# Optimization experiments

Hardware: AMD Instinct MI355X
Metric: run time of the kernel (lower is better)

## Reference

```python
import jax, jax.numpy as jnp
import numpy as np


def _gru_step(h, x, Wih, Whh, bih, bhh):
    # PyTorch GRU cell: gates ordered (r, z, n)
    gi = x @ Wih.T + bih
    gh = h @ Whh.T + bhh
    ir, iz, inn = jnp.split(gi, 3, axis=-1)
    hr, hz, hn = jnp.split(gh, 3, axis=-1)
    r = jax.nn.sigmoid(ir + hr)
    u = jax.nn.sigmoid(iz + hz)
    n = jnp.tanh(inn + r * hn)
    return (1.0 - u) * n + u * h


def _forward(mini_batch, eps, W_ih1, W_hh1, b_ih1, b_hh1, W_ih2, W_hh2, b_ih2, b_hh2,
             h1_0, h2_0, Wt1, bt1, Wloc, bloc, Wsc, bsc, We1, be1, We2, be2, We3, be3):
    B = mini_batch.shape[0]
    x_tbf = jnp.swapaxes(mini_batch, 0, 1)      # [T,B,dim_x]
    eps_tbf = jnp.swapaxes(eps, 0, 1)           # [T,B,dim_z]
    h2_init = jnp.broadcast_to(h2_0, (B, h2_0.shape[0]))
    h1_init = jnp.broadcast_to(h1_0, (B, h1_0.shape[0]))

    # gen_RNN_2 over full sequence (all seq_lengths == T, pack/pad is identity)
    def scan2(h, x):
        h = _gru_step(h, x, W_ih2, W_hh2, b_ih2, b_hh2)
        return h, h
    _, h2_seq = jax.lax.scan(scan2, h2_init, x_tbf)              # [T,B,dim_h2]
    # at step t the emitter sees h2_output[t-2] (h2_0 for t==1): shift right by one
    h2_shift = jnp.concatenate([h2_init[None], h2_seq[:-1]], axis=0)

    def step(h1, inp):
        eps_t, h2_t = inp
        # stoch_trans (dz): MLP -> z_loc, z_scale
        hid = jax.nn.relu(h1 @ Wt1.T + bt1)
        z_loc = hid @ Wloc.T + bloc
        z_scale = jax.nn.softplus(hid @ Wsc.T + bsc)
        z_t = z_loc + z_scale * eps_t                            # reparameterized sample
        h1n = _gru_step(h1, z_t, W_ih1, W_hh1, b_ih1, b_hh1)     # gen_RNN_1 one step
        dx_in = jnp.concatenate([h1n, h2_t], axis=-1)            # [B, dim_h1+dim_h2]
        e = jax.nn.relu(dx_in @ We1.T + be1)                     # emitter (dx)
        e = jax.nn.relu(e @ We2.T + be2)
        x_ps = jax.nn.sigmoid(e @ We3.T + be3)                   # Bernoulli probs
        return h1n, x_ps

    _, xps = jax.lax.scan(step, h1_init, (eps_tbf, h2_shift))    # [T,B,dim_x]
    return jnp.swapaxes(xps, 0, 1)                               # [B,T,dim_x]


def setup_inputs() -> dict:
    key = jax.random.key(0)
    B, T = 256, 1000
    DX, DZ, H1, H2, DDX, DDZ = 100, 100, 10, 10, 20, 20
    ks = jax.random.split(key, 24)
    f32 = jnp.float32
    w = lambda k, shape: (jax.random.normal(k, shape, f32) * 0.1)
    inp = {
        "mini_batch": (jax.random.uniform(ks[0], (B, T, DX)) < 0.5).astype(f32),
        "eps": jax.random.normal(ks[1], (B, T, DZ), f32),
        # gen_RNN_1: input dim_z -> hidden dim_h1
        "W_ih1": w(ks[2], (3 * H1, DZ)), "W_hh1": w(ks[3], (3 * H1, H1)),
        "b_ih1": w(ks[4], (3 * H1,)), "b_hh1": w(ks[5], (3 * H1,)),
        # gen_RNN_2: input dim_x -> hidden dim_h2
        "W_ih2": w(ks[6], (3 * H2, DX)), "W_hh2": w(ks[7], (3 * H2, H2)),
        "b_ih2": w(ks[8], (3 * H2,)), "b_hh2": w(ks[9], (3 * H2,)),
        "h1_0": jnp.zeros((H1,), f32), "h2_0": jnp.zeros((H2,), f32),
        # stoch_trans (dz): dim_h1 -> dim_dz -> (dim_z loc, dim_z scale)
        "Wt1": w(ks[10], (DDZ, H1)), "bt1": w(ks[11], (DDZ,)),
        "Wloc": w(ks[12], (DZ, DDZ)), "bloc": w(ks[13], (DZ,)),
        "Wsc": w(ks[14], (DZ, DDZ)), "bsc": w(ks[15], (DZ,)),
        # emitter (dx): (dim_h1+dim_h2) -> dim_dx -> dim_dx -> dim_x, sigmoid
        "We1": w(ks[16], (DDX, H1 + H2)), "be1": w(ks[17], (DDX,)),
        "We2": w(ks[18], (DDX, DDX)), "be2": w(ks[19], (DDX,)),
        "We3": w(ks[20], (DX, DDX)), "be3": w(ks[21], (DX,)),
    }
    return inp


def reference(mini_batch, eps, W_ih1, W_hh1, b_ih1, b_hh1, W_ih2, W_hh2, b_ih2, b_hh2,
              h1_0, h2_0, Wt1, bt1, Wloc, bloc, Wsc, bsc, We1, be1, We2, be2, We3, be3):
    return _forward(mini_batch, eps, W_ih1, W_hh1, b_ih1, b_hh1, W_ih2, W_hh2, b_ih2, b_hh2,
                    h1_0, h2_0, Wt1, bt1, Wloc, bloc, Wsc, bsc, We1, be1, We2, be2, We3, be3)
```

## Files before the change

### kernel.cpp

```cpp
#include <hip/hip_runtime.h>
#include <cstdint>

#define T_LEN 1000
#define NB    256

__device__ __forceinline__ float rcpf_(float x)     { return __builtin_amdgcn_rcpf(x); }
__device__ __forceinline__ float sigmoidf_(float x) { return rcpf_(1.f + __expf(-x)); }
__device__ __forceinline__ float tanhf_(float x) {
    float e = __expf(2.f * x);
    return 1.f - 2.f * rcpf_(e + 1.f);
}
__device__ __forceinline__ float softplusf_(float x) {
    return fmaxf(x, 0.f) + __logf(1.f + __expf(-fabsf(x)));
}
__device__ __forceinline__ float bcast_(float v, int l) {
    return __uint_as_float(__builtin_amdgcn_readlane(__float_as_uint(v), l));
}

#define BARRIER_SYNC() asm volatile("s_waitcnt lgkmcnt(0)\n\ts_barrier" ::: "memory")

__global__ __launch_bounds__(256) void gi2_kernel(
    const float* __restrict__ x, const float* __restrict__ W,
    const float* __restrict__ bias, float* __restrict__ out)
{
    __shared__ float xsT[100 * 67];

    const int tid = threadIdx.x;
    const int64_t base = (int64_t)blockIdx.x * (64 * 100);
    const float4* gx = (const float4*)(x + base);

#pragma unroll
    for (int it = 0; it < 7; ++it) {
        int i = tid + it * 256;
        if (i < 1600) {
            int r  = i / 25;
            int k4 = i - r * 25;
            float4 v = gx[i];
            xsT[(4 * k4 + 0) * 67 + r] = v.x;
            xsT[(4 * k4 + 1) * 67 + r] = v.y;
            xsT[(4 * k4 + 2) * 67 + r] = v.z;
            xsT[(4 * k4 + 3) * 67 + r] = v.w;
        }
    }
    __syncthreads();

    const int lane = tid & 63;
    const int wv   = __builtin_amdgcn_readfirstlane(tid >> 6);
    const int j0   = wv * 8;

    float acc[8];
#pragma unroll
    for (int jj = 0; jj < 8; ++jj) acc[jj] = 0.f;

    for (int k = 0; k < 100; ++k) {
        float xv = xsT[k * 67 + lane];
#pragma unroll
        for (int jj = 0; jj < 8; ++jj) {
            int j = j0 + jj; j = j > 29 ? 29 : j;
            acc[jj] = fmaf(xv, W[j * 100 + k], acc[jj]);
        }
    }
    float* orow = out + base + (int64_t)lane * 100;
#pragma unroll
    for (int jj = 0; jj < 8; ++jj) {
        int j = j0 + jj;
        if (j < 30) orow[j] = acc[jj] + bias[j];
    }
}

__global__ __launch_bounds__(128) void scan_kernel(
    const float* __restrict__ eps,
    const float* __restrict__ W_ih1, const float* __restrict__ W_hh1,
    const float* __restrict__ b_ih1, const float* __restrict__ b_hh1,
    const float* __restrict__ W_hh2, const float* __restrict__ b_hh2,
    const float* __restrict__ h1_0,  const float* __restrict__ h2_0,
    const float* __restrict__ Wt1,   const float* __restrict__ bt1,
    const float* __restrict__ Wloc,  const float* __restrict__ bloc,
    const float* __restrict__ Wsc,   const float* __restrict__ bsc,
    const float* __restrict__ We1,   const float* __restrict__ be1,
    const float* __restrict__ We2,   const float* __restrict__ be2,
    const float* __restrict__ We3,   const float* __restrict__ be3,
    float* out)
{
    __shared__ __align__(16) float ss2[2][52];
    __shared__ __align__(16) float sh1ring[2][12];

    const int lane = threadIdx.x & 63;
    const int64_t rowbase = (int64_t)blockIdx.x * T_LEN * 100;
    const int wave = __builtin_amdgcn_readfirstlane((int)(threadIdx.x >> 6));

    if (wave == 0) {
        const int j  = lane & 31;
        const int jc = j < 30 ? j : 29;
        const int h  = lane >> 5;
        const int lt = lane < 20 ? lane : 19;
        const int ls = lane < 50 ? lane : 49;

        float wt1r[10], whh1r[10], wscA[20], wscB[20], wbig[52], Cr[20];
#pragma unroll
        for (int k = 0; k < 10; ++k) {
            wt1r[k]  = Wt1[lt * 10 + k];
            whh1r[k] = W_hh1[jc * 10 + k];
        }
        float bt1r  = bt1[lt];
        float bhh1r = b_hh1[jc];
        float br1   = b_ih1[jc];
#pragma unroll
        for (int l = 0; l < 20; ++l) {
            wscA[l] = Wsc[ls * 20 + l];
            wscB[l] = Wsc[(ls + 50) * 20 + l];
        }
        float bscA = bsc[ls], bscB = bsc[ls + 50];
#pragma unroll
        for (int i = 0; i < 50; ++i) wbig[i] = W_ih1[jc * 100 + h * 50 + i];
        wbig[50] = 0.f; wbig[51] = 0.f;

        float dr = 0.f;
#pragma unroll
        for (int l = 0; l < 20; ++l) Cr[l] = 0.f;
        for (int kk = 0; kk < 100; ++kk) {
            float w = W_ih1[jc * 100 + kk];
            dr = fmaf(w, bloc[kk], dr);
#pragma unroll
            for (int l = 0; l < 20; ++l) Cr[l] = fmaf(w, Wloc[kk * 20 + l], Cr[l]);
        }

        if (lane < 2) { ss2[0][50 + lane] = 0.f; ss2[1][50 + lane] = 0.f; }

        float h1keep = h1_0[lane < 10 ? lane : 0];
        float sh1_[10];
#pragma unroll
        for (int k = 0; k < 10; ++k) sh1_[k] = h1_0[k];

        const float* erow = eps + rowbase;
        float eA0 = erow[ls],        eB0 = erow[ls + 50];
        float eA1 = erow[100 + ls],  eB1 = erow[100 + ls + 50];

#pragma unroll 1
        for (int t = 0; t <= T_LEN; ++t) {
            if (t < T_LEN) {
                const int tp = t + 2 < T_LEN ? t + 2 : T_LEN - 1;
                float eAf = erow[(int64_t)tp * 100 + ls];
                float eBf = erow[(int64_t)tp * 100 + ls + 50];

                float ha = bt1r, hb = 0.f, ga = bhh1r, gb = 0.f;
#pragma unroll
                for (int k = 0; k < 5; ++k) {
                    ha = fmaf(wt1r[2 * k],      sh1_[2 * k],     ha);
                    hb = fmaf(wt1r[2 * k + 1],  sh1_[2 * k + 1], hb);
                    ga = fmaf(whh1r[2 * k],     sh1_[2 * k],     ga);
                    gb = fmaf(whh1r[2 * k + 1], sh1_[2 * k + 1], gb);
                }
                float hidv = fmaxf(ha + hb, 0.f);
                float gh1v = ga + gb;

                float sgh[20];
#pragma unroll
                for (int l = 0; l < 20; ++l) sgh[l] = bcast_(hidv, l);

                float sA0 = bscA, sA1 = 0.f, sB0 = bscB, sB1 = 0.f, q0 = dr, q1 = 0.f;
#pragma unroll
                for (int l = 0; l < 10; ++l) {
                    sA0 = fmaf(wscA[2 * l],     sgh[2 * l],     sA0);
                    sA1 = fmaf(wscA[2 * l + 1], sgh[2 * l + 1], sA1);
                    sB0 = fmaf(wscB[2 * l],     sgh[2 * l],     sB0);
                    sB1 = fmaf(wscB[2 * l + 1], sgh[2 * l + 1], sB1);
                    q0  = fmaf(Cr[2 * l],       sgh[2 * l],     q0);
                    q1  = fmaf(Cr[2 * l + 1],   sgh[2 * l + 1], q1);
                }
                float gq = q0 + q1;
                float zA = softplusf_(sA0 + sA1) * eA0;
                float zB = softplusf_(sB0 + sB1) * eB0;
                if (lane < 50) { ss2[0][lane] = zA; ss2[1][lane] = zB; }

                eA0 = eA1; eB0 = eB1; eA1 = eAf; eB1 = eBf;

                __builtin_amdgcn_wave_barrier();

                const float4* sp4 = (const float4*)(&ss2[h][0]);
                float p0 = 0.f, p1 = 0.f, p2 = 0.f, p3 = 0.f;
#pragma unroll
                for (int c = 0; c < 13; ++c) {
                    float4 v = sp4[c];
                    p0 = fmaf(wbig[4 * c + 0], v.x, p0);
                    p1 = fmaf(wbig[4 * c + 1], v.y, p1);
                    p2 = fmaf(wbig[4 * c + 2], v.z, p2);
                    p3 = fmaf(wbig[4 * c + 3], v.w, p3);
                }
                float p = (p0 + p1) + (p2 + p3);
                float gi1v = p + __shfl_xor(p, 32) + br1 + gq;
                float av   = gi1v + gh1v;
                float a10  = __shfl(av,   lane + 10);
                float gin  = __shfl(gi1v, lane + 20);
                float ghn  = __shfl(gh1v, lane + 20);
                if (lane < 10) {
                    float r = sigmoidf_(av);
                    float u = sigmoidf_(a10);
                    float n = tanhf_(fmaf(r, ghn, gin));
                    h1keep = fmaf(u, h1keep - n, n);
                    sh1ring[t & 1][lane] = h1keep;
                }
#pragma unroll
                for (int k = 0; k < 10; ++k) sh1_[k] = bcast_(h1keep, k);
            }
            BARRIER_SYNC();
        }
    } else {
        const int lt20 = lane < 20 ? lane : 19;
        const int l30  = lane < 30 ? lane : 29;
        const int ls   = lane < 50 ? lane : 49;

        float whh2r[10];
#pragma unroll
        for (int k = 0; k < 10; ++k) whh2r[k] = W_hh2[l30 * 10 + k];
        float bhh2r = b_hh2[l30];

        float we1r[20], we2r[20], we3A[20], we3B[20];
#pragma unroll
        for (int k = 0; k < 20; ++k) {
            we1r[k] = We1[lt20 * 20 + k];
            we2r[k] = We2[lt20 * 20 + k];
            we3A[k] = We3[ls * 20 + k];
            we3B[k] = We3[(ls + 50) * 20 + k];
        }
        float be1r = be1[lt20], be2r = be2[lt20];
        float be3A = be3[ls],   be3B = be3[ls + 50];

        float h2keep = h2_0[lane < 10 ? lane : 0];
        float g2c[10], g2p[10];
#pragma unroll
        for (int k = 0; k < 10; ++k) { g2c[k] = h2_0[k]; g2p[k] = h2_0[k]; }

        float gcur = out[rowbase + l30];
        float gnxt = out[rowbase + 100 + l30];

#pragma unroll 1
        for (int t = 0; t <= T_LEN; ++t) {
            const int tp = t + 2 < T_LEN ? t + 2 : T_LEN - 1;
            float gfut = out[rowbase + (int64_t)tp * 100 + l30];

            float4 d0 = make_float4(0.f, 0.f, 0.f, 0.f);
            float4 d1 = d0; float d8 = 0.f, d9 = 0.f;
            if (t >= 1) {
                const int s1 = (t - 1) & 1;
                d0 = *(const float4*)(&sh1ring[s1][0]);
                d1 = *(const float4*)(&sh1ring[s1][4]);
                d8 = sh1ring[s1][8]; d9 = sh1ring[s1][9];
            }

            const bool upd = (t < T_LEN);
            if (upd) {
                float ga = bhh2r, gb = 0.f;
#pragma unroll
                for (int k = 0; k < 5; ++k) {
                    ga = fmaf(whh2r[2 * k],     g2c[2 * k],     ga);
                    gb = fmaf(whh2r[2 * k + 1], g2c[2 * k + 1], gb);
                }
                float gh2v = ga + gb;
                float gi2v = gcur;
                gcur = gnxt; gnxt = gfut;
                float a2  = gi2v + gh2v;
                float a10 = __shfl(a2,   lane + 10);
                float gin = __shfl(gi2v, lane + 20);
                float ghn = __shfl(gh2v, lane + 20);
                if (lane < 10) {
                    float r = sigmoidf_(a2);
                    float u = sigmoidf_(a10);
                    float n = tanhf_(fmaf(r, ghn, gin));
                    h2keep = fmaf(u, h2keep - n, n);
                }
            }

            if (t >= 1) {
                float ea = be1r, eb = 0.f;
                ea = fmaf(we1r[0], d0.x, ea); eb = fmaf(we1r[1], d0.y, eb);
                ea = fmaf(we1r[2], d0.z, ea); eb = fmaf(we1r[3], d0.w, eb);
                ea = fmaf(we1r[4], d1.x, ea); eb = fmaf(we1r[5], d1.y, eb);
                ea = fmaf(we1r[6], d1.z, ea); eb = fmaf(we1r[7], d1.w, eb);
                ea = fmaf(we1r[8], d8,   ea); eb = fmaf(we1r[9], d9,   eb);
#pragma unroll
                for (int k = 0; k < 5; ++k) {
                    ea = fmaf(we1r[10 + 2 * k],     g2p[2 * k],     ea);
                    eb = fmaf(we1r[10 + 2 * k + 1], g2p[2 * k + 1], eb);
                }
                float e1v = fmaxf(ea + eb, 0.f);

                float se1v[20];
#pragma unroll
                for (int l = 0; l < 20; ++l) se1v[l] = bcast_(e1v, l);

                float fa = be2r, fb = 0.f;
#pragma unroll
                for (int k = 0; k < 10; ++k) {
                    fa = fmaf(we2r[2 * k],     se1v[2 * k],     fa);
                    fb = fmaf(we2r[2 * k + 1], se1v[2 * k + 1], fb);
                }
                float e2v = fmaxf(fa + fb, 0.f);

                float se2v[20];
#pragma unroll
                for (int l = 0; l < 20; ++l) se2v[l] = bcast_(e2v, l);

                float xa0 = be3A, xa1 = 0.f, xb0 = be3B, xb1 = 0.f;
#pragma unroll
                for (int l = 0; l < 10; ++l) {
                    xa0 = fmaf(we3A[2 * l],     se2v[2 * l],     xa0);
                    xa1 = fmaf(we3A[2 * l + 1], se2v[2 * l + 1], xa1);
                    xb0 = fmaf(we3B[2 * l],     se2v[2 * l],     xb0);
                    xb1 = fmaf(we3B[2 * l + 1], se2v[2 * l + 1], xb1);
                }
                float xA = sigmoidf_(xa0 + xa1);
                float xB = sigmoidf_(xb0 + xb1);
                if (lane < 50) {
                    int64_t ro = rowbase + (int64_t)(t - 1) * 100;
                    out[ro + lane]      = xA;
                    out[ro + lane + 50] = xB;
                }
            }

            if (upd) {
#pragma unroll
                for (int k = 0; k < 10; ++k) g2p[k] = g2c[k];
#pragma unroll
                for (int k = 0; k < 10; ++k) g2c[k] = bcast_(h2keep, k);
            }
            BARRIER_SYNC();
        }
    }
}

extern "C" void kernel_launch(void* const* d_in, const int* in_sizes, int n_in,
                              void* d_out, int out_size, void* d_ws, size_t ws_size,
                              hipStream_t stream) {
    const float* mini_batch = (const float*)d_in[0];
    const float* eps        = (const float*)d_in[1];
    const float* W_ih1      = (const float*)d_in[2];
    const float* W_hh1      = (const float*)d_in[3];
    const float* b_ih1      = (const float*)d_in[4];
    const float* b_hh1      = (const float*)d_in[5];
    const float* W_ih2      = (const float*)d_in[6];
    const float* W_hh2      = (const float*)d_in[7];
    const float* b_ih2      = (const float*)d_in[8];
    const float* b_hh2      = (const float*)d_in[9];
    const float* h1_0       = (const float*)d_in[10];
    const float* h2_0       = (const float*)d_in[11];
    const float* Wt1        = (const float*)d_in[12];
    const float* bt1        = (const float*)d_in[13];
    const float* Wloc       = (const float*)d_in[14];
    const float* bloc       = (const float*)d_in[15];
    const float* Wsc        = (const float*)d_in[16];
    const float* bsc        = (const float*)d_in[17];
    const float* We1        = (const float*)d_in[18];
    const float* be1        = (const float*)d_in[19];
    const float* We2        = (const float*)d_in[20];
    const float* be2        = (const float*)d_in[21];
    const float* We3        = (const float*)d_in[22];
    const float* be3        = (const float*)d_in[23];
    float* out = (float*)d_out;

    gi2_kernel<<<(NB * T_LEN) / 64, 256, 0, stream>>>(mini_batch, W_ih2, b_ih2, out);

    scan_kernel<<<NB, 128, 0, stream>>>(eps, W_ih1, W_hh1, b_ih1, b_hh1, W_hh2, b_hh2,
                                        h1_0, h2_0, Wt1, bt1, Wloc, bloc, Wsc, bsc,
                                        We1, be1, We2, be2, We3, be3, out);
}
```

Measured before the change: 834.0 us.

## Add producer wave that prefetches eps and gi2 into LDS ring buffer

```diff
diff --git a/kernel.cpp b/kernel.cpp
--- a/kernel.cpp
+++ b/kernel.cpp
@@ -18,6 +18,13 @@
 }
 
 #define BARRIER_SYNC() asm volatile("s_waitcnt lgkmcnt(0)\n\ts_barrier" ::: "memory")
+
+__device__ __forceinline__ void gload_lds(const float* g, float* l) {
+    __builtin_amdgcn_global_load_lds(
+        (const __attribute__((address_space(1))) uint32_t*)g,
+        (__attribute__((address_space(3))) uint32_t*)l,
+        4, 0, 0);
+}
 
 __global__ __launch_bounds__(256) void gi2_kernel(
     const float* __restrict__ x, const float* __restrict__ W,
@@ -68,7 +75,7 @@
     }
 }
 
-__global__ __launch_bounds__(128) void scan_kernel(
+__global__ __launch_bounds__(192) void scan_kernel(
     const float* __restrict__ eps,
     const float* __restrict__ W_ih1, const float* __restrict__ W_hh1,
     const float* __restrict__ b_ih1, const float* __restrict__ b_hh1,
@@ -82,6 +89,7 @@
     const float* __restrict__ We3,   const float* __restrict__ be3,
     float* out)
 {
+    __shared__ __align__(16) float ring[4][192];
     __shared__ __align__(16) float ss2[2][52];
     __shared__ __align__(16) float sh1ring[2][12];
 
@@ -132,16 +140,14 @@
 #pragma unroll
         for (int k = 0; k < 10; ++k) sh1_[k] = h1_0[k];
 
-        const float* erow = eps + rowbase;
-        float eA0 = erow[ls],        eB0 = erow[ls + 50];
-        float eA1 = erow[100 + ls],  eB1 = erow[100 + ls + 50];
+        BARRIER_SYNC();
 
 #pragma unroll 1
         for (int t = 0; t <= T_LEN; ++t) {
             if (t < T_LEN) {
-                const int tp = t + 2 < T_LEN ? t + 2 : T_LEN - 1;
-                float eAf = erow[(int64_t)tp * 100 + ls];
-                float eBf = erow[(int64_t)tp * 100 + ls + 50];
+                const int slot = t & 3;
+                float eA = ring[slot][ls];
+                float eB = ring[slot][ls + 50];
 
                 float ha = bt1r, hb = 0.f, ga = bhh1r, gb = 0.f;
 #pragma unroll
@@ -169,11 +175,9 @@
                     q1  = fmaf(Cr[2 * l + 1],   sgh[2 * l + 1], q1);
                 }
                 float gq = q0 + q1;
-                float zA = softplusf_(sA0 + sA1) * eA0;
-                float zB = softplusf_(sB0 + sB1) * eB0;
+                float zA = softplusf_(sA0 + sA1) * eA;
+                float zB = softplusf_(sB0 + sB1) * eB;
                 if (lane < 50) { ss2[0][lane] = zA; ss2[1][lane] = zB; }
-
-                eA0 = eA1; eB0 = eB1; eA1 = eAf; eB1 = eBf;
 
                 __builtin_amdgcn_wave_barrier();
 
@@ -205,7 +209,7 @@
             }
             BARRIER_SYNC();
         }
-    } else {
+    } else if (wave == 1) {
         const int lt20 = lane < 20 ? lane : 19;
         const int l30  = lane < 30 ? lane : 29;
         const int ls   = lane < 50 ? lane : 49;
@@ -231,13 +235,13 @@
 #pragma unroll
         for (int k = 0; k < 10; ++k) { g2c[k] = h2_0[k]; g2p[k] = h2_0[k]; }
 
-        float gcur = out[rowbase + l30];
-        float gnxt = out[rowbase + 100 + l30];
+        BARRIER_SYNC();
 
 #pragma unroll 1
         for (int t = 0; t <= T_LEN; ++t) {
-            const int tp = t + 2 < T_LEN ? t + 2 : T_LEN - 1;
-            float gfut = out[rowbase + (int64_t)tp * 100 + l30];
+            const bool upd = (t < T_LEN);
+            float gi2v = 0.f;
+            if (upd) gi2v = ring[t & 3][128 + l30];
 
             float4 d0 = make_float4(0.f, 0.f, 0.f, 0.f);
             float4 d1 = d0; float d8 = 0.f, d9 = 0.f;
@@ -248,7 +252,6 @@
                 d8 = sh1ring[s1][8]; d9 = sh1ring[s1][9];
             }
 
-            const bool upd = (t < T_LEN);
             if (upd) {
                 float ga = bhh2r, gb = 0.f;
 #pragma unroll
@@ -257,8 +260,6 @@
                     gb = fmaf(whh2r[2 * k + 1], g2c[2 * k + 1], gb);
                 }
                 float gh2v = ga + gb;
-                float gi2v = gcur;
-                gcur = gnxt; gnxt = gfut;
                 float a2  = gi2v + gh2v;
                 float a10 = __shfl(a2,   lane + 10);
                 float gin = __shfl(gi2v, lane + 20);
@@ -324,6 +325,35 @@
 #pragma unroll
                 for (int k = 0; k < 10; ++k) g2c[k] = bcast_(h2keep, k);
             }
+            BARRIER_SYNC();
+        }
+    } else {
+        const float* erow = eps + rowbase;
+        const float* grow = out + rowbase;
+        const int le2 = 64 + (lane < 36 ? lane : 35);
+        const int lg  = lane < 30 ? lane : 29;
+
+#pragma unroll
+        for (int t0 = 0; t0 < 3; ++t0) {
+            const float* ep = erow + (int64_t)t0 * 100;
+            const float* gp = grow + (int64_t)t0 * 100;
+            gload_lds(ep + lane, &ring[t0][0]);
+            gload_lds(ep + le2,  &ring[t0][64]);
+            gload_lds(gp + lg,   &ring[t0][128]);
+        }
+        asm volatile("s_waitcnt vmcnt(6)" ::: "memory");
+        BARRIER_SYNC();
+
+#pragma unroll 1
+        for (int t = 0; t <= T_LEN; ++t) {
+            const int tp   = (t + 3 < T_LEN) ? t + 3 : T_LEN - 1;
+            const int slot = (t + 3) & 3;
+            const float* ep = erow + (int64_t)tp * 100;
+            const float* gp = grow + (int64_t)tp * 100;
+            gload_lds(ep + lane, &ring[slot][0]);
+            gload_lds(ep + le2,  &ring[slot][64]);
+            gload_lds(gp + lg,   &ring[slot][128]);
+            asm volatile("s_waitcnt vmcnt(6)" ::: "memory");
             BARRIER_SYNC();
         }
     }
@@ -360,7 +390,7 @@
 
     gi2_kernel<<<(NB * T_LEN) / 64, 256, 0, stream>>>(mini_batch, W_ih2, b_ih2, out);
 
-    scan_kernel<<<NB, 128, 0, stream>>>(eps, W_ih1, W_hh1, b_ih1, b_hh1, W_hh2, b_hh2,
+    scan_kernel<<<NB, 192, 0, stream>>>(eps, W_ih1, W_hh1, b_ih1, b_hh1, W_hh2, b_hh2,
                                         h1_0, h2_0, Wt1, bt1, Wloc, bloc, Wsc, bsc,
                                         We1, be1, We2, be2, We3, be3, out);
 }
```

After: 948.5 us. 13.7% more time.

## Move emitter MLP out of scan into a separate parallel kernel

Applied to the files above, without the earlier changes.

```diff
diff --git a/kernel.cpp b/kernel.cpp
--- a/kernel.cpp
+++ b/kernel.cpp
@@ -16,8 +16,6 @@
 __device__ __forceinline__ float bcast_(float v, int l) {
     return __uint_as_float(__builtin_amdgcn_readlane(__float_as_uint(v), l));
 }
-
-#define BARRIER_SYNC() asm volatile("s_waitcnt lgkmcnt(0)\n\ts_barrier" ::: "memory")
 
 __global__ __launch_bounds__(256) void gi2_kernel(
     const float* __restrict__ x, const float* __restrict__ W,
@@ -68,6 +66,102 @@
     }
 }
 
+
+#define H1_STEP(T, EA, EB, P)                                            \
+    do {                                                                 \
+        float ha = bt1r, hb = 0.f, ga = bhh1r, gb = 0.f;                 \
+        _Pragma("unroll")                                                \
+        for (int k_ = 0; k_ < 5; ++k_) {                                 \
+            ha = fmaf(wt1r[2*k_],    sh1_[2*k_],   ha);                  \
+            hb = fmaf(wt1r[2*k_+1],  sh1_[2*k_+1], hb);                  \
+            ga = fmaf(whh1r[2*k_],   sh1_[2*k_],   ga);                  \
+            gb = fmaf(whh1r[2*k_+1], sh1_[2*k_+1], gb);                  \
+        }                                                                \
+        float hidv = fmaxf(ha + hb, 0.f);                                \
+        float gh1v = ga + gb;                                            \
+        float sgh[20];                                                   \
+        _Pragma("unroll")                                                \
+        for (int l_ = 0; l_ < 20; ++l_) sgh[l_] = bcast_(hidv, l_);      \
+        float sA0 = bscA, sA1 = 0.f, sB0 = bscB, sB1 = 0.f;              \
+        float q0 = dr, q1 = 0.f;                                         \
+        _Pragma("unroll")                                                \
+        for (int l_ = 0; l_ < 10; ++l_) {                                \
+            sA0 = fmaf(wscA[2*l_],   sgh[2*l_],   sA0);                  \
+            sA1 = fmaf(wscA[2*l_+1], sgh[2*l_+1], sA1);                  \
+            sB0 = fmaf(wscB[2*l_],   sgh[2*l_],   sB0);                  \
+            sB1 = fmaf(wscB[2*l_+1], sgh[2*l_+1], sB1);                  \
+            q0  = fmaf(Cr[2*l_],     sgh[2*l_],   q0);                   \
+            q1  = fmaf(Cr[2*l_+1],   sgh[2*l_+1], q1);                   \
+        }                                                                \
+        float gq = q0 + q1;                                              \
+        float zA = softplusf_(sA0 + sA1) * (EA);                         \
+        float zB = softplusf_(sB0 + sB1) * (EB);                         \
+        if (lane < 50) { ss2[P][lane] = zA; ss2[P][52 + lane] = zB; }    \
+        {             \
+            int tp_ = (T) + 2 < T_LEN ? (T) + 2 : (T);                   \
+            const float* ep_ = erow + (int64_t)tp_ * 100;                \
+            (EA) = ep_[ls]; (EB) = ep_[ls + 50];                         \
+        }                                                                \
+        __builtin_amdgcn_wave_barrier();                                 \
+        {                                                                \
+            const float4* sp4_ = (const float4*)(&ss2[P][52 * h]);       \
+            float p0 = 0.f, p1 = 0.f, p2 = 0.f, p3 = 0.f;                \
+            _Pragma("unroll")                                            \
+            for (int c_ = 0; c_ < 13; ++c_) {                            \
+                float4 v_ = sp4_[c_];                                    \
+                p0 = fmaf(wbig[4*c_+0], v_.x, p0);                       \
+                p1 = fmaf(wbig[4*c_+1], v_.y, p1);                       \
+                p2 = fmaf(wbig[4*c_+2], v_.z, p2);                       \
+                p3 = fmaf(wbig[4*c_+3], v_.w, p3);                       \
+            }                                                            \
+            float p_ = (p0 + p1) + (p2 + p3);                            \
+            float gi1v = p_ + __shfl_xor(p_, 32) + br1 + gq;             \
+            float av   = gi1v + gh1v;                                    \
+            float a10  = __shfl(av,   lane + 10);                        \
+            float gin  = __shfl(gi1v, lane + 20);                        \
+            float ghn  = __shfl(gh1v, lane + 20);                        \
+            if (lane < 10) {                                             \
+                float r_ = sigmoidf_(av);                                \
+                float u_ = sigmoidf_(a10);                               \
+                float n_ = tanhf_(fmaf(r_, ghn, gin));                   \
+                h1keep = fmaf(u_, h1keep - n_, n_);                      \
+                out[rowbase + (int64_t)(T) * 100 + 30 + lane] = h1keep;  \
+            }                                                            \
+        }                                                                \
+        _Pragma("unroll")                                                \
+        for (int k_ = 0; k_ < 10; ++k_) sh1_[k_] = bcast_(h1keep, k_);   \
+    } while (0)
+
+#define H2_STEP(T, GC)                                                   \
+    do {                                                                 \
+        if (lane < 10)                 \
+            out[rowbase + (int64_t)(T) * 100 + 40 + lane] = h2keep;      \
+        float ga = bhh2r, gb = 0.f;                                      \
+        _Pragma("unroll")                                                \
+        for (int k_ = 0; k_ < 5; ++k_) {                                 \
+            ga = fmaf(whh2r[2*k_],   g2c[2*k_],   ga);                   \
+            gb = fmaf(whh2r[2*k_+1], g2c[2*k_+1], gb);                   \
+        }                                                                \
+        float gh2v = ga + gb;                                            \
+        float gi2v = (GC);                                               \
+        {                                         \
+            int tp_ = (T) + 2 < T_LEN ? (T) + 2 : (T);                   \
+            (GC) = out[rowbase + (int64_t)tp_ * 100 + l30];              \
+        }                                                                \
+        float a2  = gi2v + gh2v;                                         \
+        float a10 = __shfl(a2,   lane + 10);                             \
+        float gin = __shfl(gi2v, lane + 20);                             \
+        float ghn = __shfl(gh2v, lane + 20);                             \
+        if (lane < 10) {                                                 \
+            float r_ = sigmoidf_(a2);                                    \
+            float u_ = sigmoidf_(a10);                                   \
+            float n_ = tanhf_(fmaf(r_, ghn, gin));                       \
+            h2keep = fmaf(u_, h2keep - n_, n_);                          \
+        }                                                                \
+        _Pragma("unroll")                                                \
+        for (int k_ = 0; k_ < 10; ++k_) g2c[k_] = bcast_(h2keep, k_);    \
+    } while (0)
+
 __global__ __launch_bounds__(128) void scan_kernel(
     const float* __restrict__ eps,
     const float* __restrict__ W_ih1, const float* __restrict__ W_hh1,
@@ -77,13 +171,9 @@
     const float* __restrict__ Wt1,   const float* __restrict__ bt1,
     const float* __restrict__ Wloc,  const float* __restrict__ bloc,
     const float* __restrict__ Wsc,   const float* __restrict__ bsc,
-    const float* __restrict__ We1,   const float* __restrict__ be1,
-    const float* __restrict__ We2,   const float* __restrict__ be2,
-    const float* __restrict__ We3,   const float* __restrict__ be3,
     float* out)
 {
-    __shared__ __align__(16) float ss2[2][52];
-    __shared__ __align__(16) float sh1ring[2][12];
+    __shared__ __align__(16) float ss2[2][104];
 
     const int lane = threadIdx.x & 63;
     const int64_t rowbase = (int64_t)blockIdx.x * T_LEN * 100;
@@ -125,7 +215,10 @@
             for (int l = 0; l < 20; ++l) Cr[l] = fmaf(w, Wloc[kk * 20 + l], Cr[l]);
         }
 
-        if (lane < 2) { ss2[0][50 + lane] = 0.f; ss2[1][50 + lane] = 0.f; }
+        if (lane < 2) {
+            ss2[0][50 + lane] = 0.f; ss2[0][102 + lane] = 0.f;
+            ss2[1][50 + lane] = 0.f; ss2[1][102 + lane] = 0.f;
+        }
 
         float h1keep = h1_0[lane < 10 ? lane : 0];
         float sh1_[10];
@@ -137,194 +230,105 @@
         float eA1 = erow[100 + ls],  eB1 = erow[100 + ls + 50];
 
 #pragma unroll 1
-        for (int t = 0; t <= T_LEN; ++t) {
-            if (t < T_LEN) {
-                const int tp = t + 2 < T_LEN ? t + 2 : T_LEN - 1;
-                float eAf = erow[(int64_t)tp * 100 + ls];
-                float eBf = erow[(int64_t)tp * 100 + ls + 50];
-
-                float ha = bt1r, hb = 0.f, ga = bhh1r, gb = 0.f;
-#pragma unroll
-                for (int k = 0; k < 5; ++k) {
-                    ha = fmaf(wt1r[2 * k],      sh1_[2 * k],     ha);
-                    hb = fmaf(wt1r[2 * k + 1],  sh1_[2 * k + 1], hb);
-                    ga = fmaf(whh1r[2 * k],     sh1_[2 * k],     ga);
-                    gb = fmaf(whh1r[2 * k + 1], sh1_[2 * k + 1], gb);
-                }
-                float hidv = fmaxf(ha + hb, 0.f);
-                float gh1v = ga + gb;
-
-                float sgh[20];
-#pragma unroll
-                for (int l = 0; l < 20; ++l) sgh[l] = bcast_(hidv, l);
-
-                float sA0 = bscA, sA1 = 0.f, sB0 = bscB, sB1 = 0.f, q0 = dr, q1 = 0.f;
-#pragma unroll
-                for (int l = 0; l < 10; ++l) {
-                    sA0 = fmaf(wscA[2 * l],     sgh[2 * l],     sA0);
-                    sA1 = fmaf(wscA[2 * l + 1], sgh[2 * l + 1], sA1);
-                    sB0 = fmaf(wscB[2 * l],     sgh[2 * l],     sB0);
-                    sB1 = fmaf(wscB[2 * l + 1], sgh[2 * l + 1], sB1);
-                    q0  = fmaf(Cr[2 * l],       sgh[2 * l],     q0);
-                    q1  = fmaf(Cr[2 * l + 1],   sgh[2 * l + 1], q1);
-                }
-                float gq = q0 + q1;
-                float zA = softplusf_(sA0 + sA1) * eA0;
-                float zB = softplusf_(sB0 + sB1) * eB0;
-                if (lane < 50) { ss2[0][lane] = zA; ss2[1][lane] = zB; }
-
-                eA0 = eA1; eB0 = eB1; eA1 = eAf; eB1 = eBf;
-
-                __builtin_amdgcn_wave_barrier();
-
-                const float4* sp4 = (const float4*)(&ss2[h][0]);
-                float p0 = 0.f, p1 = 0.f, p2 = 0.f, p3 = 0.f;
-#pragma unroll
-                for (int c = 0; c < 13; ++c) {
-                    float4 v = sp4[c];
-                    p0 = fmaf(wbig[4 * c + 0], v.x, p0);
-                    p1 = fmaf(wbig[4 * c + 1], v.y, p1);
-                    p2 = fmaf(wbig[4 * c + 2], v.z, p2);
-                    p3 = fmaf(wbig[4 * c + 3], v.w, p3);
-                }
-                float p = (p0 + p1) + (p2 + p3);
-                float gi1v = p + __shfl_xor(p, 32) + br1 + gq;
-                float av   = gi1v + gh1v;
-                float a10  = __shfl(av,   lane + 10);
-                float gin  = __shfl(gi1v, lane + 20);
-                float ghn  = __shfl(gh1v, lane + 20);
-                if (lane < 10) {
-                    float r = sigmoidf_(av);
-                    float u = sigmoidf_(a10);
-                    float n = tanhf_(fmaf(r, ghn, gin));
-                    h1keep = fmaf(u, h1keep - n, n);
-                    sh1ring[t & 1][lane] = h1keep;
-                }
-#pragma unroll
-                for (int k = 0; k < 10; ++k) sh1_[k] = bcast_(h1keep, k);
-            }
-            BARRIER_SYNC();
+        for (int t = 0; t < T_LEN; t += 2) {
+            H1_STEP(t,     eA0, eB0, 0);
+            H1_STEP(t + 1, eA1, eB1, 1);
         }
     } else {
-        const int lt20 = lane < 20 ? lane : 19;
-        const int l30  = lane < 30 ? lane : 29;
-        const int ls   = lane < 50 ? lane : 49;
+        const int l30 = lane < 30 ? lane : 29;
 
         float whh2r[10];
 #pragma unroll
         for (int k = 0; k < 10; ++k) whh2r[k] = W_hh2[l30 * 10 + k];
         float bhh2r = b_hh2[l30];
 
-        float we1r[20], we2r[20], we3A[20], we3B[20];
-#pragma unroll
-        for (int k = 0; k < 20; ++k) {
-            we1r[k] = We1[lt20 * 20 + k];
-            we2r[k] = We2[lt20 * 20 + k];
-            we3A[k] = We3[ls * 20 + k];
-            we3B[k] = We3[(ls + 50) * 20 + k];
-        }
-        float be1r = be1[lt20], be2r = be2[lt20];
-        float be3A = be3[ls],   be3B = be3[ls + 50];
-
         float h2keep = h2_0[lane < 10 ? lane : 0];
-        float g2c[10], g2p[10];
-#pragma unroll
-        for (int k = 0; k < 10; ++k) { g2c[k] = h2_0[k]; g2p[k] = h2_0[k]; }
-
-        float gcur = out[rowbase + l30];
-        float gnxt = out[rowbase + 100 + l30];
+        float g2c[10];
+#pragma unroll
+        for (int k = 0; k < 10; ++k) g2c[k] = h2_0[k];
+
+        float gU = out[rowbase + l30];
+        float gV = out[rowbase + 100 + l30];
 
 #pragma unroll 1
-        for (int t = 0; t <= T_LEN; ++t) {
-            const int tp = t + 2 < T_LEN ? t + 2 : T_LEN - 1;
-            float gfut = out[rowbase + (int64_t)tp * 100 + l30];
-
-            float4 d0 = make_float4(0.f, 0.f, 0.f, 0.f);
-            float4 d1 = d0; float d8 = 0.f, d9 = 0.f;
-            if (t >= 1) {
-                const int s1 = (t - 1) & 1;
-                d0 = *(const float4*)(&sh1ring[s1][0]);
-                d1 = *(const float4*)(&sh1ring[s1][4]);
-                d8 = sh1ring[s1][8]; d9 = sh1ring[s1][9];
-            }
-
-            const bool upd = (t < T_LEN);
-            if (upd) {
-                float ga = bhh2r, gb = 0.f;
-#pragma unroll
-                for (int k = 0; k < 5; ++k) {
-                    ga = fmaf(whh2r[2 * k],     g2c[2 * k],     ga);
-                    gb = fmaf(whh2r[2 * k + 1], g2c[2 * k + 1], gb);
-                }
-                float gh2v = ga + gb;
-                float gi2v = gcur;
-                gcur = gnxt; gnxt = gfut;
-                float a2  = gi2v + gh2v;
-                float a10 = __shfl(a2,   lane + 10);
-                float gin = __shfl(gi2v, lane + 20);
-                float ghn = __shfl(gh2v, lane + 20);
-                if (lane < 10) {
-                    float r = sigmoidf_(a2);
-                    float u = sigmoidf_(a10);
-                    float n = tanhf_(fmaf(r, ghn, gin));
-                    h2keep = fmaf(u, h2keep - n, n);
-                }
-            }
-
-            if (t >= 1) {
-                float ea = be1r, eb = 0.f;
-                ea = fmaf(we1r[0], d0.x, ea); eb = fmaf(we1r[1], d0.y, eb);
-                ea = fmaf(we1r[2], d0.z, ea); eb = fmaf(we1r[3], d0.w, eb);
-                ea = fmaf(we1r[4], d1.x, ea); eb = fmaf(we1r[5], d1.y, eb);
-                ea = fmaf(we1r[6], d1.z, ea); eb = fmaf(we1r[7], d1.w, eb);
-                ea = fmaf(we1r[8], d8,   ea); eb = fmaf(we1r[9], d9,   eb);
-#pragma unroll
-                for (int k = 0; k < 5; ++k) {
-                    ea = fmaf(we1r[10 + 2 * k],     g2p[2 * k],     ea);
-                    eb = fmaf(we1r[10 + 2 * k + 1], g2p[2 * k + 1], eb);
-                }
-                float e1v = fmaxf(ea + eb, 0.f);
-
-                float se1v[20];
-#pragma unroll
-                for (int l = 0; l < 20; ++l) se1v[l] = bcast_(e1v, l);
-
-                float fa = be2r, fb = 0.f;
-#pragma unroll
-                for (int k = 0; k < 10; ++k) {
-                    fa = fmaf(we2r[2 * k],     se1v[2 * k],     fa);
-                    fb = fmaf(we2r[2 * k + 1], se1v[2 * k + 1], fb);
-                }
-                float e2v = fmaxf(fa + fb, 0.f);
-
-                float se2v[20];
-#pragma unroll
-                for (int l = 0; l < 20; ++l) se2v[l] = bcast_(e2v, l);
-
-                float xa0 = be3A, xa1 = 0.f, xb0 = be3B, xb1 = 0.f;
-#pragma unroll
-                for (int l = 0; l < 10; ++l) {
-                    xa0 = fmaf(we3A[2 * l],     se2v[2 * l],     xa0);
-                    xa1 = fmaf(we3A[2 * l + 1], se2v[2 * l + 1], xa1);
-                    xb0 = fmaf(we3B[2 * l],     se2v[2 * l],     xb0);
-                    xb1 = fmaf(we3B[2 * l + 1], se2v[2 * l + 1], xb1);
-                }
-                float xA = sigmoidf_(xa0 + xa1);
-                float xB = sigmoidf_(xb0 + xb1);
-                if (lane < 50) {
-                    int64_t ro = rowbase + (int64_t)(t - 1) * 100;
-                    out[ro + lane]      = xA;
-                    out[ro + lane + 50] = xB;
-                }
-            }
-
-            if (upd) {
-#pragma unroll
-                for (int k = 0; k < 10; ++k) g2p[k] = g2c[k];
-#pragma unroll
-                for (int k = 0; k < 10; ++k) g2c[k] = bcast_(h2keep, k);
-            }
-            BARRIER_SYNC();
+        for (int t = 0; t < T_LEN; t += 2) {
+            H2_STEP(t,     gU);
+            H2_STEP(t + 1, gV);
+        }
+    }
+}
+
+__global__ __launch_bounds__(256) void emit_kernel(
+    const float* __restrict__ We1, const float* __restrict__ be1,
+    const float* __restrict__ We2, const float* __restrict__ be2,
+    const float* __restrict__ We3, const float* __restrict__ be3,
+    float* out)
+{
+    const int lane = threadIdx.x & 63;
+    const int wid  = threadIdx.x >> 6;
+    const int lt = lane < 20 ? lane : 19;
+    const int ls = lane < 50 ? lane : 49;
+
+    float we1r[20], we2r[20], we3A[20], we3B[20];
+#pragma unroll
+    for (int k = 0; k < 20; ++k) {
+        we1r[k] = We1[lt * 20 + k];
+        we2r[k] = We2[lt * 20 + k];
+        we3A[k] = We3[ls * 20 + k];
+        we3B[k] = We3[(ls + 50) * 20 + k];
+    }
+    float be1r = be1[lt], be2r = be2[lt];
+    float be3A = be3[ls], be3B = be3[ls + 50];
+
+    const int64_t row0 = ((int64_t)blockIdx.x * 4 + wid) * 8;
+
+#pragma unroll 1
+    for (int rr = 0; rr < 8; ++rr) {
+        const int64_t r = row0 + rr;
+        float hvin = 0.f;
+        if (lane < 20) hvin = out[r * 100 + 30 + lane];
+
+        float hall[20];
+#pragma unroll
+        for (int l = 0; l < 20; ++l) hall[l] = bcast_(hvin, l);
+
+        float ea = be1r, eb = 0.f;
+#pragma unroll
+        for (int k = 0; k < 10; ++k) {
+            ea = fmaf(we1r[2 * k],     hall[2 * k],     ea);
+            eb = fmaf(we1r[2 * k + 1], hall[2 * k + 1], eb);
+        }
+        float e1v = fmaxf(ea + eb, 0.f);
+
+        float se1[20];
+#pragma unroll
+        for (int l = 0; l < 20; ++l) se1[l] = bcast_(e1v, l);
+
+        float fa = be2r, fb = 0.f;
+#pragma unroll
+        for (int k = 0; k < 10; ++k) {
+            fa = fmaf(we2r[2 * k],     se1[2 * k],     fa);
+            fb = fmaf(we2r[2 * k + 1], se1[2 * k + 1], fb);
+        }
+        float e2v = fmaxf(fa + fb, 0.f);
+
+        float se2[20];
+#pragma unroll
+        for (int l = 0; l < 20; ++l) se2[l] = bcast_(e2v, l);
+
+        float xa0 = be3A, xa1 = 0.f, xb0 = be3B, xb1 = 0.f;
+#pragma unroll
+        for (int l = 0; l < 10; ++l) {
+            xa0 = fmaf(we3A[2 * l],     se2[2 * l],     xa0);
+            xa1 = fmaf(we3A[2 * l + 1], se2[2 * l + 1], xa1);
+            xb0 = fmaf(we3B[2 * l],     se2[2 * l],     xb0);
+            xb1 = fmaf(we3B[2 * l + 1], se2[2 * l + 1], xb1);
+        }
+        float xA = sigmoidf_(xa0 + xa1);
+        float xB = sigmoidf_(xb0 + xb1);
+        if (lane < 50) {
+            out[r * 100 + lane]      = xA;
+            out[r * 100 + lane + 50] = xB;
         }
     }
 }
@@ -361,6 +365,7 @@
     gi2_kernel<<<(NB * T_LEN) / 64, 256, 0, stream>>>(mini_batch, W_ih2, b_ih2, out);
 
     scan_kernel<<<NB, 128, 0, stream>>>(eps, W_ih1, W_hh1, b_ih1, b_hh1, W_hh2, b_hh2,
-                                        h1_0, h2_0, Wt1, bt1, Wloc, bloc, Wsc, bsc,
-                                        We1, be1, We2, be2, We3, be3, out);
-}
+                                        h1_0, h2_0, Wt1, bt1, Wloc, bloc, Wsc, bsc, out);
+
+    emit_kernel<<<(NB * T_LEN) / 32, 256, 0, stream>>>(We1, be1, We2, be2, We3, be3, out);
+}
```

Result: no change. 832.8 us (-0.1%).

## Unroll GRU scan by two, shorten critical path with permlane swap and earlier sigmoid

Applied to the files above, without the earlier changes.

```diff
diff --git a/kernel.cpp b/kernel.cpp
--- a/kernel.cpp
+++ b/kernel.cpp
@@ -16,8 +16,12 @@
 __device__ __forceinline__ float bcast_(float v, int l) {
     return __uint_as_float(__builtin_amdgcn_readlane(__float_as_uint(v), l));
 }
-
-#define BARRIER_SYNC() asm volatile("s_waitcnt lgkmcnt(0)\n\ts_barrier" ::: "memory")
+__device__ __forceinline__ float halfsum_(float p) {
+    float a = p, b = p;
+    asm volatile("s_nop 1\n\tv_permlane32_swap_b32 %0, %1\n\ts_nop 1"
+                 : "+v"(a), "+v"(b));
+    return a + b;
+}
 
 __global__ __launch_bounds__(256) void gi2_kernel(
     const float* __restrict__ x, const float* __restrict__ W,
@@ -67,6 +71,86 @@
         if (j < 30) orow[j] = acc[jj] + bias[j];
     }
 }
+
+
+#define H1_STEP(T, EA, EB)                                               \
+    do {                                                                 \
+                                                \
+        float ha = bt1r, hb = 0.f;                                       \
+        _Pragma("unroll")                                                \
+        for (int k_ = 0; k_ < 5; ++k_) {                                 \
+            ha = fmaf(wt1r[2*k_],   sh1_[2*k_],   ha);                   \
+            hb = fmaf(wt1r[2*k_+1], sh1_[2*k_+1], hb);                   \
+        }                                                                \
+        float hidv = fmaxf(ha + hb, 0.f);                                \
+        float sgh[20];                                                   \
+        _Pragma("unroll")                                                \
+        for (int l_ = 0; l_ < 20; ++l_) sgh[l_] = bcast_(hidv, l_);      \
+                          \
+        float sA0 = bscA, sA1 = 0.f, sA2 = 0.f, sA3 = 0.f;               \
+        float sB0 = bscB, sB1 = 0.f, sB2 = 0.f, sB3 = 0.f;               \
+        float q0 = dr, q1 = 0.f, q2 = 0.f, q3 = 0.f;                     \
+        _Pragma("unroll")                                                \
+        for (int l_ = 0; l_ < 5; ++l_) {                                 \
+            sA0 = fmaf(wscA[4*l_],   sgh[4*l_],   sA0);                  \
+            sA1 = fmaf(wscA[4*l_+1], sgh[4*l_+1], sA1);                  \
+            sA2 = fmaf(wscA[4*l_+2], sgh[4*l_+2], sA2);                  \
+            sA3 = fmaf(wscA[4*l_+3], sgh[4*l_+3], sA3);                  \
+            sB0 = fmaf(wscB[4*l_],   sgh[4*l_],   sB0);                  \
+            sB1 = fmaf(wscB[4*l_+1], sgh[4*l_+1], sB1);                  \
+            sB2 = fmaf(wscB[4*l_+2], sgh[4*l_+2], sB2);                  \
+            sB3 = fmaf(wscB[4*l_+3], sgh[4*l_+3], sB3);                  \
+            q0  = fmaf(Cr[4*l_],     sgh[4*l_],   q0);                   \
+            q1  = fmaf(Cr[4*l_+1],   sgh[4*l_+1], q1);                   \
+            q2  = fmaf(Cr[4*l_+2],   sgh[4*l_+2], q2);                   \
+            q3  = fmaf(Cr[4*l_+3],   sgh[4*l_+3], q3);                   \
+        }                                                                \
+        float gq = (q0 + q1) + (q2 + q3);                                \
+        float zA = softplusf_((sA0 + sA1) + (sA2 + sA3)) * (EA);         \
+        float zB = softplusf_((sB0 + sB1) + (sB2 + sB3)) * (EB);         \
+        if (lane < 50) { ss2[lane] = zA; ss2[52 + lane] = zB; }          \
+          \
+        float ga = bhh1r, gb = 0.f;                                      \
+        _Pragma("unroll")                                                \
+        for (int k_ = 0; k_ < 5; ++k_) {                                 \
+            ga = fmaf(whh1r[2*k_],   sh1_[2*k_],   ga);                  \
+            gb = fmaf(whh1r[2*k_+1], sh1_[2*k_+1], gb);                  \
+        }                                                                \
+        float gh1v = ga + gb;                                            \
+        {                                                                \
+            int tp_ = (T) + 2 < T_LEN ? (T) + 2 : (T);                   \
+            const float* ep_ = erow + (int64_t)tp_ * 100;                \
+            (EA) = ep_[ls]; (EB) = ep_[ls + 50];                         \
+        }                                                                \
+        __builtin_amdgcn_wave_barrier();                                 \
+           \
+        {                                                                \
+            const float4* sp4_ = (const float4*)(&ss2[52 * h]);          \
+            float p0 = 0.f, p1 = 0.f, p2 = 0.f, p3 = 0.f;                \
+            _Pragma("unroll")                                            \
+            for (int c_ = 0; c_ < 13; ++c_) {                            \
+                float4 v_ = sp4_[c_];                                    \
+                p0 = fmaf(wbig[4*c_+0], v_.x, p0);                       \
+                p1 = fmaf(wbig[4*c_+1], v_.y, p1);                       \
+                p2 = fmaf(wbig[4*c_+2], v_.z, p2);                       \
+                p3 = fmaf(wbig[4*c_+3], v_.w, p3);                       \
+            }                                                            \
+            float p_ = (p0 + p1) + (p2 + p3);                            \
+            float gi1v = halfsum_(p_) + br1 + gq;                        \
+            float av   = gi1v + gh1v;                                    \
+            float sg   = sigmoidf_(av);          \
+            float su   = __shfl(sg,   lane + 10);                        \
+            float gin  = __shfl(gi1v, lane + 20);                        \
+            float ghn  = __shfl(gh1v, lane + 20);                        \
+            if (lane < 10) {                                             \
+                float n_ = tanhf_(fmaf(sg, ghn, gin));                   \
+                h1keep = fmaf(su, h1keep - n_, n_);                      \
+                sh1ring[(T) & 1][lane] = h1keep;           \
+            }                                                            \
+        }                                                                \
+        _Pragma("unroll")                                                \
+        for (int k_ = 0; k_ < 10; ++k_) sh1_[k_] = bcast_(h1keep, k_);   \
+    } while (0)
 
 __global__ __launch_bounds__(128) void scan_kernel(
     const float* __restrict__ eps,
@@ -82,7 +166,7 @@
     const float* __restrict__ We3,   const float* __restrict__ be3,
     float* out)
 {
-    __shared__ __align__(16) float ss2[2][52];
+    __shared__ __align__(16) float ss2[104];
     __shared__ __align__(16) float sh1ring[2][12];
 
     const int lane = threadIdx.x & 63;
@@ -125,7 +209,7 @@
             for (int l = 0; l < 20; ++l) Cr[l] = fmaf(w, Wloc[kk * 20 + l], Cr[l]);
         }
 
-        if (lane < 2) { ss2[0][50 + lane] = 0.f; ss2[1][50 + lane] = 0.f; }
+        if (lane < 2) { ss2[50 + lane] = 0.f; ss2[102 + lane] = 0.f; }
 
         float h1keep = h1_0[lane < 10 ? lane : 0];
         float sh1_[10];
@@ -137,74 +221,13 @@
         float eA1 = erow[100 + ls],  eB1 = erow[100 + ls + 50];
 
 #pragma unroll 1
-        for (int t = 0; t <= T_LEN; ++t) {
-            if (t < T_LEN) {
-                const int tp = t + 2 < T_LEN ? t + 2 : T_LEN - 1;
-                float eAf = erow[(int64_t)tp * 100 + ls];
-                float eBf = erow[(int64_t)tp * 100 + ls + 50];
-
-                float ha = bt1r, hb = 0.f, ga = bhh1r, gb = 0.f;
-#pragma unroll
-                for (int k = 0; k < 5; ++k) {
-                    ha = fmaf(wt1r[2 * k],      sh1_[2 * k],     ha);
-                    hb = fmaf(wt1r[2 * k + 1],  sh1_[2 * k + 1], hb);
-                    ga = fmaf(whh1r[2 * k],     sh1_[2 * k],     ga);
-                    gb = fmaf(whh1r[2 * k + 1], sh1_[2 * k + 1], gb);
-                }
-                float hidv = fmaxf(ha + hb, 0.f);
-                float gh1v = ga + gb;
-
-                float sgh[20];
-#pragma unroll
-                for (int l = 0; l < 20; ++l) sgh[l] = bcast_(hidv, l);
-
-                float sA0 = bscA, sA1 = 0.f, sB0 = bscB, sB1 = 0.f, q0 = dr, q1 = 0.f;
-#pragma unroll
-                for (int l = 0; l < 10; ++l) {
-                    sA0 = fmaf(wscA[2 * l],     sgh[2 * l],     sA0);
-                    sA1 = fmaf(wscA[2 * l + 1], sgh[2 * l + 1], sA1);
-                    sB0 = fmaf(wscB[2 * l],     sgh[2 * l],     sB0);
-                    sB1 = fmaf(wscB[2 * l + 1], sgh[2 * l + 1], sB1);
-                    q0  = fmaf(Cr[2 * l],       sgh[2 * l],     q0);
-                    q1  = fmaf(Cr[2 * l + 1],   sgh[2 * l + 1], q1);
-                }
-                float gq = q0 + q1;
-                float zA = softplusf_(sA0 + sA1) * eA0;
-                float zB = softplusf_(sB0 + sB1) * eB0;
-                if (lane < 50) { ss2[0][lane] = zA; ss2[1][lane] = zB; }
-
-                eA0 = eA1; eB0 = eB1; eA1 = eAf; eB1 = eBf;
-
-                __builtin_amdgcn_wave_barrier();
-
-                const float4* sp4 = (const float4*)(&ss2[h][0]);
-                float p0 = 0.f, p1 = 0.f, p2 = 0.f, p3 = 0.f;
-#pragma unroll
-                for (int c = 0; c < 13; ++c) {
-                    float4 v = sp4[c];
-                    p0 = fmaf(wbig[4 * c + 0], v.x, p0);
-                    p1 = fmaf(wbig[4 * c + 1], v.y, p1);
-                    p2 = fmaf(wbig[4 * c + 2], v.z, p2);
-                    p3 = fmaf(wbig[4 * c + 3], v.w, p3);
-                }
-                float p = (p0 + p1) + (p2 + p3);
-                float gi1v = p + __shfl_xor(p, 32) + br1 + gq;
-                float av   = gi1v + gh1v;
-                float a10  = __shfl(av,   lane + 10);
-                float gin  = __shfl(gi1v, lane + 20);
-                float ghn  = __shfl(gh1v, lane + 20);
-                if (lane < 10) {
-                    float r = sigmoidf_(av);
-                    float u = sigmoidf_(a10);
-                    float n = tanhf_(fmaf(r, ghn, gin));
-                    h1keep = fmaf(u, h1keep - n, n);
-                    sh1ring[t & 1][lane] = h1keep;
-                }
-#pragma unroll
-                for (int k = 0; k < 10; ++k) sh1_[k] = bcast_(h1keep, k);
-            }
-            BARRIER_SYNC();
-        }
+        for (int t = 0; t < T_LEN; t += 2) {
+            H1_STEP(t, eA0, eB0);
+            __syncthreads();
+            H1_STEP(t + 1, eA1, eB1);
+            __syncthreads();
+        }
+        __syncthreads();
     } else {
         const int lt20 = lane < 20 ? lane : 19;
         const int l30  = lane < 30 ? lane : 29;
@@ -236,8 +259,7 @@
 
 #pragma unroll 1
         for (int t = 0; t <= T_LEN; ++t) {
-            const int tp = t + 2 < T_LEN ? t + 2 : T_LEN - 1;
-            float gfut = out[rowbase + (int64_t)tp * 100 + l30];
+            const bool upd = (t < T_LEN);
 
             float4 d0 = make_float4(0.f, 0.f, 0.f, 0.f);
             float4 d1 = d0; float d8 = 0.f, d9 = 0.f;
@@ -248,7 +270,6 @@
                 d8 = sh1ring[s1][8]; d9 = sh1ring[s1][9];
             }
 
-            const bool upd = (t < T_LEN);
             if (upd) {
                 float ga = bhh2r, gb = 0.f;
 #pragma unroll
@@ -258,16 +279,19 @@
                 }
                 float gh2v = ga + gb;
                 float gi2v = gcur;
-                gcur = gnxt; gnxt = gfut;
+                gcur = gnxt;
+                {
+                    int tp = t + 2 < T_LEN ? t + 2 : T_LEN - 1;
+                    gnxt = out[rowbase + (int64_t)tp * 100 + l30];
+                }
                 float a2  = gi2v + gh2v;
-                float a10 = __shfl(a2,   lane + 10);
+                float sg2 = sigmoidf_(a2);
+                float su  = __shfl(sg2,  lane + 10);
                 float gin = __shfl(gi2v, lane + 20);
                 float ghn = __shfl(gh2v, lane + 20);
                 if (lane < 10) {
-                    float r = sigmoidf_(a2);
-                    float u = sigmoidf_(a10);
-                    float n = tanhf_(fmaf(r, ghn, gin));
-                    h2keep = fmaf(u, h2keep - n, n);
+                    float n_ = tanhf_(fmaf(sg2, ghn, gin));
+                    h2keep = fmaf(su, h2keep - n_, n_);
                 }
             }
 
@@ -324,7 +348,7 @@
 #pragma unroll
                 for (int k = 0; k < 10; ++k) g2c[k] = bcast_(h2keep, k);
             }
-            BARRIER_SYNC();
+            __syncthreads();
         }
     }
 }
```

After: 802.4 us. 3.8% less time.
